# Kernel tuning notes

Measured on AMD Instinct MI355X. Metric: run time of the kernel, lower is better.

## Reference

```python
import jax, jax.numpy as jnp
import numpy as np

SOS = 1

def _gru_cell(x, h, Wih, Whh, bih, bhh):
    # PyTorch GRU cell: gates ordered (r, z, n)
    gi = x @ Wih.T + bih
    gh = h @ Whh.T + bhh
    ir, iz, inn = jnp.split(gi, 3, axis=-1)
    hr, hz, hn = jnp.split(gh, 3, axis=-1)
    r = jax.nn.sigmoid(ir + hr)
    z = jax.nn.sigmoid(iz + hz)
    n = jnp.tanh(inn + r * hn)
    return (1.0 - z) * n + z * h


def setup_inputs() -> dict:
    key = jax.random.key(0)
    ks = jax.random.split(key, 17)
    V, E, H, Lin, Tout, B, Lmax = 50000, 512, 512, 400, 100, 64, 400
    s = 0.05
    f = jax.random.normal
    return {
        "emb":     f(ks[0], (V, E)) * s,
        "enc_Wih": f(ks[1], (3 * H, E)) * s,
        "enc_Whh": f(ks[2], (3 * H, H)) * s,
        "enc_bih": f(ks[3], (3 * H,)) * s,
        "enc_bhh": f(ks[4], (3 * H,)) * s,
        "attn_W":  f(ks[5], (Lmax, 2 * H)) * s,
        "attn_b":  f(ks[6], (Lmax,)) * s,
        "comb_W":  f(ks[7], (H, 2 * H)) * s,
        "comb_b":  f(ks[8], (H,)) * s,
        "dec_Wih": f(ks[9], (3 * H, H)) * s,
        "dec_Whh": f(ks[10], (3 * H, H)) * s,
        "dec_bih": f(ks[11], (3 * H,)) * s,
        "dec_bhh": f(ks[12], (3 * H,)) * s,
        "out_W":   f(ks[13], (V, H)) * s,
        "out_b":   f(ks[14], (V,)) * s,
        "input_tensor":  jax.random.randint(ks[15], (Lin, B), 0, V),
        "target_tensor": jax.random.randint(ks[16], (Tout, B), 0, V),
    }


def reference(emb, enc_Wih, enc_Whh, enc_bih, enc_bhh, attn_W, attn_b,
              comb_W, comb_b, dec_Wih, dec_Whh, dec_bih, dec_bhh,
              out_W, out_b, input_tensor, target_tensor):
    B = input_tensor.shape[1]
    H = enc_Whh.shape[1]

    # ---- encoder: 1-layer GRU over [L, B, E] ----
    enc_x = emb[input_tensor]                      # [L, B, E]
    h0 = jnp.zeros((B, H), enc_x.dtype)
    def enc_step(h, x):
        h2 = _gru_cell(x, h, enc_Wih, enc_Whh, enc_bih, enc_bhh)
        return h2, h2
    h_enc, enc_out = jax.lax.scan(enc_step, h0, enc_x)   # enc_out: [L, B, H]
    enc0 = enc_out[0]                              # [B, H]; source's attn_applied[0] picks timestep 0

    # ---- decoder: teacher-forced, NLLLoss(mean) summed over steps ----
    dec_tokens = jnp.concatenate(
        [jnp.full((1, B), SOS, target_tensor.dtype), target_tensor[:-1]], axis=0)
    dec_x = emb[dec_tokens]                        # [T, B, H] (embed_size == hidden_size)

    def dec_step(h, xt):
        x, tgt = xt                                # x: [B, H], tgt: [B]
        a = jax.nn.softmax(jnp.concatenate([x, h], 1) @ attn_W.T + attn_b, axis=1)  # [B, Lmax]
        # faithful to source: elementwise broadcast picks enc_out[0] scaled by a[:, 0]
        ctx = enc0 * a[:, :1]                      # [B, H]
        c = jax.nn.relu(jnp.concatenate([x, ctx], 1) @ comb_W.T + comb_b)           # [B, H]
        h2 = _gru_cell(c, h, dec_Wih, dec_Whh, dec_bih, dec_bhh)
        logp = jax.nn.log_softmax(h2 @ out_W.T + out_b, axis=1)                     # [B, V]
        loss_t = -jnp.mean(jnp.take_along_axis(logp, tgt[:, None], axis=1))
        return h2, loss_t

    _, losses = jax.lax.scan(dec_step, h_enc, (dec_x, target_tensor))
    return jnp.sum(losses)
```

## Files before the change

### kernel.cpp

```cpp
#include <hip/hip_runtime.h>
#include <math.h>


typedef __attribute__((ext_vector_type(8))) short bh8;
typedef __attribute__((ext_vector_type(4))) float fv4;

__device__ __forceinline__ float b2f(short u) {
    union { unsigned int i; float f; } c;
    c.i = ((unsigned int)(unsigned short)u) << 16;
    return c.f;
}
__device__ __forceinline__ short f2b(float f) {
    union { float f; unsigned int u; } c;
    c.f = f;
    unsigned int r = (c.u + 0x7fffu + ((c.u >> 16) & 1u)) >> 16;
    return (short)r;
}
__device__ __forceinline__ bh8 ld8(const float* __restrict__ p) {
    bh8 r;
    #pragma unroll
    for (int j = 0; j < 8; ++j) r[j] = f2b(p[j]);
    return r;
}
__device__ __forceinline__ float sigmf(float x) { return 1.f / (1.f + expf(-x)); }

__device__ __forceinline__ fv4 mfma16(bh8 a, bh8 b, fv4 c) {
    return __builtin_amdgcn_mfma_f32_16x16x32_bf16(a, b, c, 0, 0, 0);
}

__device__ __forceinline__ void gridbar(unsigned int* bar, unsigned int target) {
    __syncthreads();
    if (threadIdx.x == 0) {
        __hip_atomic_fetch_add(bar, 1u, __ATOMIC_ACQ_REL, __HIP_MEMORY_SCOPE_AGENT);
        while (__hip_atomic_load(bar, __ATOMIC_ACQUIRE, __HIP_MEMORY_SCOPE_AGENT) < target) {
            __builtin_amdgcn_s_sleep(2);
        }
    }
    __syncthreads();
}

__global__ __launch_bounds__(256) void k_cvt(
    const float* __restrict__ s, short* __restrict__ d, int n)
{
    const int i = (blockIdx.x * 256 + threadIdx.x) * 4;
    if (i + 3 < n) {
        fv4 v = *(const fv4*)(s + i);
        short4 o;
        o.x = f2b(v[0]); o.y = f2b(v[1]); o.z = f2b(v[2]); o.w = f2b(v[3]);
        *(short4*)(d + i) = o;
    }
}

__global__ __launch_bounds__(256) void k_enc_persist(
    const float* __restrict__ emb, const int* __restrict__ input_t,
    const short* __restrict__ Wb,
    const float* __restrict__ Wih_f, const float* __restrict__ Whh_f,
    const float* __restrict__ bih, const float* __restrict__ bhh,
    float* __restrict__ h_f32, short* __restrict__ h_bf,
    float* __restrict__ enc0, unsigned int* __restrict__ bar)
{
    const int tid  = threadIdx.x;
    const int lane = tid & 63;
    const int wv   = tid >> 6;
    const int n0   = blockIdx.x * 16;
    const int b0   = wv * 16;
    const int l15  = lane & 15;
    const int ko   = lane >> 4;
    const int koff = ko * 8;
    const int brow = b0 + l15;
    const int n    = n0 + l15;

    for (int i = blockIdx.x * 256 + tid; i < 64 * 512; i += 32 * 256) {
        h_f32[i] = 0.f; h_bf[i] = 0;
    }
    gridbar(bar, 32u);

    const bh8 *Wrb = nullptr, *Wzb = nullptr, *Wnb = nullptr;
    const bh8 *Urb = nullptr, *Uzb = nullptr, *Unb = nullptr;
    const float *Wrf = nullptr, *Wzf = nullptr, *Wnf = nullptr;
    const float *Urf = nullptr, *Uzf = nullptr, *Unf = nullptr;
    if (Wb) {
        Wrb = (const bh8*)(Wb + (long long)(n + 0)    * 512) + ko;
        Wzb = (const bh8*)(Wb + (long long)(n + 512)  * 512) + ko;
        Wnb = (const bh8*)(Wb + (long long)(n + 1024) * 512) + ko;
        Urb = (const bh8*)(Wb + (long long)(n + 1536) * 512) + ko;
        Uzb = (const bh8*)(Wb + (long long)(n + 2048) * 512) + ko;
        Unb = (const bh8*)(Wb + (long long)(n + 2560) * 512) + ko;
    } else {
        Wrf = Wih_f + (long long)(n + 0)    * 512 + koff;
        Wzf = Wih_f + (long long)(n + 512)  * 512 + koff;
        Wnf = Wih_f + (long long)(n + 1024) * 512 + koff;
        Urf = Whh_f + (long long)(n + 0)    * 512 + koff;
        Uzf = Whh_f + (long long)(n + 512)  * 512 + koff;
        Unf = Whh_f + (long long)(n + 1024) * 512 + koff;
    }
    const float bir = bih[n], biz = bih[n + 512], bin = bih[n + 1024];
    const float bhr = bhh[n], bhz = bhh[n + 512], bhn = bhh[n + 1024];

    for (int t = 0; t < 400; ++t) {
        const float* hi  = h_f32 + (t & 1) * 32768;
        const short* hib = h_bf  + (t & 1) * 32768;
        float* ho  = h_f32 + ((t + 1) & 1) * 32768;
        short* hob = h_bf  + ((t + 1) & 1) * 32768;

        const int tok = input_t[t * 64 + brow];
        const float* Ap = emb + (long long)tok * 512 + koff;
        const bh8*  Hp  = (const bh8*)(hib + (long long)brow * 512) + ko;

        fv4 air = {0.f, 0.f, 0.f, 0.f};
        fv4 aiz = air, ain = air, ahr = air, ahz = air, ahn = air;
        if (Wb) {
            #pragma unroll 4
            for (int kk = 0; kk < 16; ++kk) {
                const bh8 a = ld8(Ap + kk * 32);
                const bh8 h = Hp[kk * 4];
                air = mfma16(a, Wrb[kk * 4], air);
                aiz = mfma16(a, Wzb[kk * 4], aiz);
                ain = mfma16(a, Wnb[kk * 4], ain);
                ahr = mfma16(h, Urb[kk * 4], ahr);
                ahz = mfma16(h, Uzb[kk * 4], ahz);
                ahn = mfma16(h, Unb[kk * 4], ahn);
            }
        } else {
            #pragma unroll 4
            for (int kk = 0; kk < 16; ++kk) {
                const bh8 a = ld8(Ap + kk * 32);
                const bh8 h = Hp[kk * 4];
                air = mfma16(a, ld8(Wrf + kk * 32), air);
                aiz = mfma16(a, ld8(Wzf + kk * 32), aiz);
                ain = mfma16(a, ld8(Wnf + kk * 32), ain);
                ahr = mfma16(h, ld8(Urf + kk * 32), ahr);
                ahz = mfma16(h, ld8(Uzf + kk * 32), ahz);
                ahn = mfma16(h, ld8(Unf + kk * 32), ahn);
            }
        }
        #pragma unroll
        for (int r = 0; r < 4; ++r) {
            const int b = b0 + ko * 4 + r;
            const float rr = sigmf(air[r] + bir + ahr[r] + bhr);
            const float zz = sigmf(aiz[r] + biz + ahz[r] + bhz);
            const float nn = tanhf(ain[r] + bin + rr * (ahn[r] + bhn));
            const float hold = hi[b * 512 + n];
            const float hnew = (1.f - zz) * nn + zz * hold;
            ho[b * 512 + n] = hnew;
            hob[b * 512 + n] = f2b(hnew);
            if (t == 0) enc0[b * 512 + n] = hnew;
        }
        gridbar(bar, 32u * (t + 2));
    }
}

__global__ __launch_bounds__(256) void k_gru1(
    const short* __restrict__ c_bf, const short* __restrict__ Wb,
    const float* __restrict__ Wih_f, const float* __restrict__ Whh_f,
    const float* __restrict__ bih, const float* __restrict__ bhh,
    const float* __restrict__ hi, const short* __restrict__ hib,
    float* __restrict__ ho, short* __restrict__ hob)
{
    const int tid  = threadIdx.x;
    const int lane = tid & 63;
    const int w    = blockIdx.x * 4 + (tid >> 6);
    const int b0   = (w & 3) * 16;
    const int n0   = (w >> 2) * 16;
    const int l15  = lane & 15;
    const int ko   = lane >> 4;
    const int koff = ko * 8;
    const int brow = b0 + l15;
    const int n    = n0 + l15;

    const bh8* Ap = (const bh8*)(c_bf + (long long)brow * 512) + ko;
    const bh8* Hp = (const bh8*)(hib + (long long)brow * 512) + ko;

    fv4 air = {0.f, 0.f, 0.f, 0.f};
    fv4 aiz = air, ain = air, ahr = air, ahz = air, ahn = air;
    if (Wb) {
        const bh8* Wr = (const bh8*)(Wb + (long long)(n + 0)    * 512) + ko;
        const bh8* Wz = (const bh8*)(Wb + (long long)(n + 512)  * 512) + ko;
        const bh8* Wn = (const bh8*)(Wb + (long long)(n + 1024) * 512) + ko;
        const bh8* Ur = (const bh8*)(Wb + (long long)(n + 1536) * 512) + ko;
        const bh8* Uz = (const bh8*)(Wb + (long long)(n + 2048) * 512) + ko;
        const bh8* Un = (const bh8*)(Wb + (long long)(n + 2560) * 512) + ko;
        #pragma unroll 4
        for (int kk = 0; kk < 16; ++kk) {
            const bh8 a = Ap[kk * 4];
            const bh8 h = Hp[kk * 4];
            air = mfma16(a, Wr[kk * 4], air);
            aiz = mfma16(a, Wz[kk * 4], aiz);
            ain = mfma16(a, Wn[kk * 4], ain);
            ahr = mfma16(h, Ur[kk * 4], ahr);
            ahz = mfma16(h, Uz[kk * 4], ahz);
            ahn = mfma16(h, Un[kk * 4], ahn);
        }
    } else {
        const float* Wr = Wih_f + (long long)(n + 0)    * 512 + koff;
        const float* Wz = Wih_f + (long long)(n + 512)  * 512 + koff;
        const float* Wn = Wih_f + (long long)(n + 1024) * 512 + koff;
        const float* Ur = Whh_f + (long long)(n + 0)    * 512 + koff;
        const float* Uz = Whh_f + (long long)(n + 512)  * 512 + koff;
        const float* Un = Whh_f + (long long)(n + 1024) * 512 + koff;
        #pragma unroll 4
        for (int kk = 0; kk < 16; ++kk) {
            const bh8 a = Ap[kk * 4];
            const bh8 h = Hp[kk * 4];
            air = mfma16(a, ld8(Wr + kk * 32), air);
            aiz = mfma16(a, ld8(Wz + kk * 32), aiz);
            ain = mfma16(a, ld8(Wn + kk * 32), ain);
            ahr = mfma16(h, ld8(Ur + kk * 32), ahr);
            ahz = mfma16(h, ld8(Uz + kk * 32), ahz);
            ahn = mfma16(h, ld8(Un + kk * 32), ahn);
        }
    }
    const float bir = bih[n], biz = bih[n + 512], bin = bih[n + 1024];
    const float bhr = bhh[n], bhz = bhh[n + 512], bhn = bhh[n + 1024];
    #pragma unroll
    for (int r = 0; r < 4; ++r) {
        const int b = b0 + ko * 4 + r;
        const float rr = sigmf(air[r] + bir + ahr[r] + bhr);
        const float zz = sigmf(aiz[r] + biz + ahz[r] + bhz);
        const float nn = tanhf(ain[r] + bin + rr * (ahn[r] + bhn));
        const float hold = hi[b * 512 + n];
        const float hnew = (1.f - zz) * nn + zz * hold;
        ho[b * 512 + n] = hnew;
        hob[b * 512 + n] = f2b(hnew);
    }
}

__global__ __launch_bounds__(256) void k_attncomb(
    const float* __restrict__ emb, const float* __restrict__ h_f32,
    const float* __restrict__ enc0,
    const float* __restrict__ attn_W, const float* __restrict__ attn_b,
    const float* __restrict__ comb_W, const float* __restrict__ comb_b,
    const int* __restrict__ target, int td, short* __restrict__ c_bf)
{
    __shared__ float sx[1024];
    __shared__ float sc[400];
    __shared__ float red[256];
    __shared__ float a0s;
    const int b = blockIdx.x;
    const int tid = threadIdx.x;
    const int tok = (td == 0) ? 1 : target[(td - 1) * 64 + b];
    for (int k = tid; k < 512; k += 256) {
        sx[k] = emb[(long long)tok * 512 + k];
        sx[512 + k] = h_f32[b * 512 + k];
    }
    __syncthreads();
    for (int nn = tid; nn < 400; nn += 256) {
        const fv4* wrow = (const fv4*)(attn_W + (long long)nn * 1024);
        float acc = 0.f;
        for (int kc = 0; kc < 256; ++kc) {
            fv4 v = wrow[kc];
            acc += v[0] * sx[kc * 4 + 0] + v[1] * sx[kc * 4 + 1]
                 + v[2] * sx[kc * 4 + 2] + v[3] * sx[kc * 4 + 3];
        }
        sc[nn] = acc + attn_b[nn];
    }
    __syncthreads();
    float m = -1e30f;
    for (int nn = tid; nn < 400; nn += 256) m = fmaxf(m, sc[nn]);
    red[tid] = m;
    __syncthreads();
    for (int s = 128; s > 0; s >>= 1) {
        if (tid < s) red[tid] = fmaxf(red[tid], red[tid + s]);
        __syncthreads();
    }
    m = red[0];
    __syncthreads();
    float ss = 0.f;
    for (int nn = tid; nn < 400; nn += 256) ss += expf(sc[nn] - m);
    red[tid] = ss;
    __syncthreads();
    for (int s = 128; s > 0; s >>= 1) {
        if (tid < s) red[tid] += red[tid + s];
        __syncthreads();
    }
    if (tid == 0) a0s = expf(sc[0] - m) / red[0];
    __syncthreads();
    const float a0b = a0s;
    for (int k = tid; k < 512; k += 256) sx[512 + k] = enc0[b * 512 + k] * a0b;
    __syncthreads();
    for (int j = tid; j < 512; j += 256) {
        const fv4* wrow = (const fv4*)(comb_W + (long long)j * 1024);
        float acc = 0.f;
        for (int kc = 0; kc < 256; ++kc) {
            fv4 v = wrow[kc];
            acc += v[0] * sx[kc * 4 + 0] + v[1] * sx[kc * 4 + 1]
                 + v[2] * sx[kc * 4 + 2] + v[3] * sx[kc * 4 + 3];
        }
        acc += comb_b[j];
        c_bf[b * 512 + j] = f2b(fmaxf(acc, 0.f));
    }
}

__global__ __launch_bounds__(256) void k_outloss(
    const short* __restrict__ h2bf,
    const short* __restrict__ outWb, const float* __restrict__ outW,
    const float* __restrict__ outb, const int* __restrict__ target,
    float* __restrict__ pm, float* __restrict__ ps, float* __restrict__ tlogit)
{
    __shared__ float sl[64][65];
    const int tid  = threadIdx.x;
    const int lane = tid & 63;
    const int wl   = tid >> 6;
    const int base = blockIdx.x * 64;
    const int n0   = base + wl * 16;
    const int l15  = lane & 15;
    const int ko   = lane >> 4;

    const int v    = n0 + l15;
    const int vcl  = (v < 50000) ? v : 49999;
    const bh8* A0 = (const bh8*)(h2bf + (long long)(0  + l15) * 512) + ko;
    const bh8* A1 = (const bh8*)(h2bf + (long long)(16 + l15) * 512) + ko;
    const bh8* A2 = (const bh8*)(h2bf + (long long)(32 + l15) * 512) + ko;
    const bh8* A3 = (const bh8*)(h2bf + (long long)(48 + l15) * 512) + ko;
    fv4 c0 = {0.f, 0.f, 0.f, 0.f};
    fv4 c1 = c0, c2 = c0, c3 = c0;
    if (outWb) {
        const bh8* Bp = (const bh8*)(outWb + (long long)vcl * 512) + ko;
        #pragma unroll 4
        for (int kk = 0; kk < 16; ++kk) {
            const bh8 bb = Bp[kk * 4];
            c0 = mfma16(A0[kk * 4], bb, c0);
            c1 = mfma16(A1[kk * 4], bb, c1);
            c2 = mfma16(A2[kk * 4], bb, c2);
            c3 = mfma16(A3[kk * 4], bb, c3);
        }
    } else {
        const float* Bp = outW + (long long)vcl * 512 + ko * 8;
        #pragma unroll 4
        for (int kk = 0; kk < 16; ++kk) {
            const bh8 bb = ld8(Bp + kk * 32);
            c0 = mfma16(A0[kk * 4], bb, c0);
            c1 = mfma16(A1[kk * 4], bb, c1);
            c2 = mfma16(A2[kk * 4], bb, c2);
            c3 = mfma16(A3[kk * 4], bb, c3);
        }
    }
    const float bv = outb[vcl];
    const int cc = wl * 16 + l15;
    const bool ok = (v < 50000);
    #pragma unroll
    for (int r = 0; r < 4; ++r) {
        const int row = ko * 4 + r;
        sl[0  + row][cc] = ok ? (c0[r] + bv) : -1e30f;
        sl[16 + row][cc] = ok ? (c1[r] + bv) : -1e30f;
        sl[32 + row][cc] = ok ? (c2[r] + bv) : -1e30f;
        sl[48 + row][cc] = ok ? (c3[r] + bv) : -1e30f;
    }
    __syncthreads();
    if (tid < 64) {
        const int b = tid;
        float m = -1e30f, s = 0.f;
        for (int c = 0; c < 64; ++c) {
            const float x = sl[b][c];
            if (x > m) { s = s * expf(m - x) + 1.f; m = x; }
            else       { s += expf(x - m); }
        }
        pm[blockIdx.x * 64 + b] = m;
        ps[blockIdx.x * 64 + b] = s;
        const int tg = target[b];
        const int rel = tg - base;
        if (rel >= 0 && rel < 64) tlogit[b] = sl[b][rel];
    }
}

__global__ __launch_bounds__(256) void k_lossred(
    const float* __restrict__ pm, const float* __restrict__ ps,
    const float* __restrict__ tlogit, float* __restrict__ loss_acc)
{
    __shared__ float rm[256], rs[256];
    const int b = blockIdx.x;
    const int tid = threadIdx.x;
    float m = -1e30f, s = 0.f;
    for (int i = tid; i < 782; i += 256) {
        const float m2 = pm[i * 64 + b];
        const float s2 = ps[i * 64 + b];
        if (m2 > m) { s = s * expf(m - m2) + s2; m = m2; }
        else        { s += s2 * expf(m2 - m); }
    }
    rm[tid] = m; rs[tid] = s;
    __syncthreads();
    for (int st = 128; st > 0; st >>= 1) {
        if (tid < st) {
            const float m2 = rm[tid + st], s2 = rs[tid + st];
            const float M = fmaxf(rm[tid], m2);
            rs[tid] = rs[tid] * expf(rm[tid] - M) + s2 * expf(m2 - M);
            rm[tid] = M;
        }
        __syncthreads();
    }
    if (tid == 0) {
        const float logp = tlogit[b] - (rm[0] + logf(rs[0]));
        atomicAdd(loss_acc, -logp * (1.f / 64.f));
    }
}

__global__ void k_init(float* h_f32_0, short* h_bf_0, float* loss_acc,
                       unsigned int* bar)
{
    const int i = blockIdx.x * 256 + threadIdx.x;
    if (i < 64 * 512) { h_f32_0[i] = 0.f; h_bf_0[i] = 0; }
    if (i == 0) { *loss_acc = 0.f; *bar = 0u; }
}

__global__ void k_final(const float* loss_acc, float* out)
{
    out[0] = *loss_acc;
}

extern "C" void kernel_launch(void* const* d_in, const int* in_sizes, int n_in,
                              void* d_out, int out_size, void* d_ws, size_t ws_size,
                              hipStream_t stream)
{
    const float* emb     = (const float*)d_in[0];
    const float* enc_Wih = (const float*)d_in[1];
    const float* enc_Whh = (const float*)d_in[2];
    const float* enc_bih = (const float*)d_in[3];
    const float* enc_bhh = (const float*)d_in[4];
    const float* attn_W  = (const float*)d_in[5];
    const float* attn_b  = (const float*)d_in[6];
    const float* comb_W  = (const float*)d_in[7];
    const float* comb_b  = (const float*)d_in[8];
    const float* dec_Wih = (const float*)d_in[9];
    const float* dec_Whh = (const float*)d_in[10];
    const float* dec_bih = (const float*)d_in[11];
    const float* dec_bhh = (const float*)d_in[12];
    const float* out_W   = (const float*)d_in[13];
    const float* out_b   = (const float*)d_in[14];
    const int*   input_t = (const int*)d_in[15];
    const int*   target_t= (const int*)d_in[16];

    char* ws = (char*)d_ws;
    float* h_f32  = (float*)(ws + 0);
    float* enc0   = (float*)(ws + 262144);
    short* h_bf   = (short*)(ws + 393216);
    short* c_bf   = (short*)(ws + 524288);
    float* lacc   = (float*)(ws + 589824);
    unsigned int* bar = (unsigned int*)(ws + 590080);
    float* pm     = (float*)(ws + 590336);
    float* ps     = (float*)(ws + 790528);
    float* tlog   = (float*)(ws + 990720);
    short* encWb  = (short*)(ws + 990976);
    short* decWb  = (short*)(ws + 4136704);
    short* outWb  = (short*)(ws + 7282432);

    const bool tier1 = ws_size >= 7282432;
    const bool tier2 = ws_size >= 58482432;

    k_init<<<128, 256, 0, stream>>>(h_f32, h_bf, lacc, bar);

    if (tier1) {
        k_cvt<<<768, 256, 0, stream>>>(enc_Wih, encWb, 786432);
        k_cvt<<<768, 256, 0, stream>>>(enc_Whh, encWb + 786432, 786432);
        k_cvt<<<768, 256, 0, stream>>>(dec_Wih, decWb, 786432);
        k_cvt<<<768, 256, 0, stream>>>(dec_Whh, decWb + 786432, 786432);
    }
    if (tier2) {
        k_cvt<<<25000, 256, 0, stream>>>(out_W, outWb, 25600000);
    }

    k_enc_persist<<<32, 256, 0, stream>>>(
        emb, input_t, tier1 ? encWb : nullptr, enc_Wih, enc_Whh,
        enc_bih, enc_bhh, h_f32, h_bf, enc0, bar);

    for (int td = 0; td < 100; ++td) {
        const float* hi  = h_f32 + (td & 1) * 32768;
        const short* hib = h_bf  + (td & 1) * 32768;
        float* ho  = h_f32 + ((td + 1) & 1) * 32768;
        short* hob = h_bf  + ((td + 1) & 1) * 32768;
        k_attncomb<<<64, 256, 0, stream>>>(emb, hi, enc0, attn_W, attn_b,
                                           comb_W, comb_b, target_t, td, c_bf);
        k_gru1<<<32, 256, 0, stream>>>(c_bf, tier1 ? decWb : nullptr,
                                       dec_Wih, dec_Whh, dec_bih, dec_bhh,
                                       hi, hib, ho, hob);
        k_outloss<<<782, 256, 0, stream>>>(hob, tier2 ? outWb : nullptr, out_W,
                                           out_b, target_t + td * 64,
                                           pm, ps, tlog);
        k_lossred<<<64, 256, 0, stream>>>(pm, ps, tlog, lacc);
    }

    k_final<<<1, 1, 0, stream>>>(lacc, (float*)d_out);
}
```

Baseline: 28.86 ms.

## Fuse decoder steps into a single persistent kernel with grid barriers

Replaces the per-step launches of the attention/combine, GRU, output-projection and loss-reduction kernels with one persistent 256-block kernel that loops over all 100 decoder steps, separating phases with grid-wide barriers. The loss reduction of step t is folded into the start of step t+1, and attention scores are staged in reused workspace. This removes hundreds of kernel launches and their gaps, at the cost of fewer blocks per phase and a dependence on all blocks being co-resident for the barriers.

```diff
diff --git a/kernel.cpp b/kernel.cpp
--- a/kernel.cpp
+++ b/kernel.cpp
@@ -148,6 +148,272 @@
         }
         gridbar(bar, 32u * (t + 2));
     }
+}
+
+struct SmAB { float sx[1024]; float red[256]; float red2[256]; };
+struct SmD  { float sl[64][65]; };
+union SMem { SmAB ab; SmD d; };
+
+__device__ __forceinline__ void dec_lossred(
+    const float* __restrict__ pm, const float* __restrict__ ps,
+    const float* __restrict__ tlog, float* __restrict__ lacc,
+    float* red, float* red2, int r, int tid)
+{
+    float m = -1e30f, s = 0.f;
+    for (int i = tid; i < 782; i += 256) {
+        const float m2 = pm[i * 64 + r];
+        const float s2 = ps[i * 64 + r];
+        if (m2 > m) { s = s * expf(m - m2) + s2; m = m2; }
+        else        { s += s2 * expf(m2 - m); }
+    }
+    red[tid] = m; red2[tid] = s;
+    __syncthreads();
+    for (int st = 128; st > 0; st >>= 1) {
+        if (tid < st) {
+            const float m2 = red[tid + st], s2 = red2[tid + st];
+            const float M = fmaxf(red[tid], m2);
+            red2[tid] = red2[tid] * expf(red[tid] - M) + s2 * expf(m2 - M);
+            red[tid] = M;
+        }
+        __syncthreads();
+    }
+    if (tid == 0) {
+        const float logp = tlog[r] - (red[0] + logf(red2[0]));
+        atomicAdd(lacc, -logp * (1.f / 64.f));
+    }
+    __syncthreads();
+}
+
+__global__ __launch_bounds__(256) void k_dec_persist(
+    const float* __restrict__ emb, const float* __restrict__ enc0,
+    const float* __restrict__ attn_W, const float* __restrict__ attn_b,
+    const float* __restrict__ comb_W, const float* __restrict__ comb_b,
+    const short* __restrict__ decWb,
+    const float* __restrict__ dec_Wih, const float* __restrict__ dec_Whh,
+    const float* __restrict__ dec_bih, const float* __restrict__ dec_bhh,
+    const short* __restrict__ outWb, const float* __restrict__ outW,
+    const float* __restrict__ outb, const int* __restrict__ target,
+    float* __restrict__ h_f32, short* __restrict__ h_bf,
+    short* __restrict__ c_bf, float* __restrict__ scores,
+    float* __restrict__ pm, float* __restrict__ ps,
+    float* __restrict__ tlog, float* __restrict__ lacc,
+    unsigned int* __restrict__ bar2)
+{
+    __shared__ SMem sm;
+    const int tid = threadIdx.x;
+    const int bid = blockIdx.x;
+    const int r   = bid >> 2;
+    const int q   = bid & 3;
+    unsigned int tgt = 0u;
+
+    for (int t = 0; t < 100; ++t) {
+        const float* hi  = h_f32 + (t & 1) * 32768;
+        const short* hib = h_bf  + (t & 1) * 32768;
+        float* ho  = h_f32 + ((t + 1) & 1) * 32768;
+        short* hob = h_bf  + ((t + 1) & 1) * 32768;
+
+        const int tok = (t == 0) ? 1 : target[(t - 1) * 64 + r];
+        for (int k = tid; k < 512; k += 256) {
+            sm.ab.sx[k]       = emb[(long long)tok * 512 + k];
+            sm.ab.sx[512 + k] = hi[r * 512 + k];
+        }
+        if (q == 0 && t > 0)
+            dec_lossred(pm, ps, tlog, lacc, sm.ab.red, sm.ab.red2, r, tid);
+        __syncthreads();
+        if (tid < 100) {
+            const int nn = q * 100 + tid;
+            const fv4* wrow = (const fv4*)(attn_W + (long long)nn * 1024);
+            float s0 = 0.f, s1 = 0.f, s2 = 0.f, s3 = 0.f;
+            for (int kc = 0; kc < 256; ++kc) {
+                fv4 v = wrow[kc];
+                s0 += v[0] * sm.ab.sx[kc * 4 + 0];
+                s1 += v[1] * sm.ab.sx[kc * 4 + 1];
+                s2 += v[2] * sm.ab.sx[kc * 4 + 2];
+                s3 += v[3] * sm.ab.sx[kc * 4 + 3];
+            }
+            scores[r * 400 + nn] = (s0 + s1) + (s2 + s3) + attn_b[nn];
+        }
+        tgt += 256u; gridbar(bar2, tgt);
+
+        {
+            float m = -1e30f;
+            for (int i = tid; i < 400; i += 256) m = fmaxf(m, scores[r * 400 + i]);
+            sm.ab.red[tid] = m;
+            __syncthreads();
+            for (int st = 128; st > 0; st >>= 1) {
+                if (tid < st) sm.ab.red[tid] = fmaxf(sm.ab.red[tid], sm.ab.red[tid + st]);
+                __syncthreads();
+            }
+            m = sm.ab.red[0];
+            __syncthreads();
+            float ssum = 0.f;
+            for (int i = tid; i < 400; i += 256) ssum += expf(scores[r * 400 + i] - m);
+            sm.ab.red2[tid] = ssum;
+            __syncthreads();
+            for (int st = 128; st > 0; st >>= 1) {
+                if (tid < st) sm.ab.red2[tid] += sm.ab.red2[tid + st];
+                __syncthreads();
+            }
+            const float a0 = expf(scores[r * 400 + 0] - m) / sm.ab.red2[0];
+            __syncthreads();
+            for (int k = tid; k < 512; k += 256)
+                sm.ab.sx[512 + k] = enc0[r * 512 + k] * a0;
+            __syncthreads();
+        }
+        if (tid < 128) {
+            const int j = q * 128 + tid;
+            const fv4* wrow = (const fv4*)(comb_W + (long long)j * 1024);
+            float s0 = 0.f, s1 = 0.f, s2 = 0.f, s3 = 0.f;
+            for (int kc = 0; kc < 256; ++kc) {
+                fv4 v = wrow[kc];
+                s0 += v[0] * sm.ab.sx[kc * 4 + 0];
+                s1 += v[1] * sm.ab.sx[kc * 4 + 1];
+                s2 += v[2] * sm.ab.sx[kc * 4 + 2];
+                s3 += v[3] * sm.ab.sx[kc * 4 + 3];
+            }
+            const float acc = (s0 + s1) + (s2 + s3) + comb_b[j];
+            c_bf[r * 512 + j] = f2b(fmaxf(acc, 0.f));
+        }
+        tgt += 256u; gridbar(bar2, tgt);
+
+        if (bid < 32) {
+            const int lane = tid & 63;
+            const int w    = bid * 4 + (tid >> 6);
+            const int b0g  = (w & 3) * 16;
+            const int n0g  = (w >> 2) * 16;
+            const int l15  = lane & 15;
+            const int ko   = lane >> 4;
+            const int koff = ko * 8;
+            const int brow = b0g + l15;
+            const int n    = n0g + l15;
+
+            const bh8* Ap = (const bh8*)(c_bf + (long long)brow * 512) + ko;
+            const bh8* Hp = (const bh8*)(hib + (long long)brow * 512) + ko;
+
+            fv4 air = {0.f, 0.f, 0.f, 0.f};
+            fv4 aiz = air, ain = air, ahr = air, ahz = air, ahn = air;
+            if (decWb) {
+                const bh8* Wr = (const bh8*)(decWb + (long long)(n + 0)    * 512) + ko;
+                const bh8* Wz = (const bh8*)(decWb + (long long)(n + 512)  * 512) + ko;
+                const bh8* Wn = (const bh8*)(decWb + (long long)(n + 1024) * 512) + ko;
+                const bh8* Ur = (const bh8*)(decWb + (long long)(n + 1536) * 512) + ko;
+                const bh8* Uz = (const bh8*)(decWb + (long long)(n + 2048) * 512) + ko;
+                const bh8* Un = (const bh8*)(decWb + (long long)(n + 2560) * 512) + ko;
+                #pragma unroll 4
+                for (int kk = 0; kk < 16; ++kk) {
+                    const bh8 a = Ap[kk * 4];
+                    const bh8 h = Hp[kk * 4];
+                    air = mfma16(a, Wr[kk * 4], air);
+                    aiz = mfma16(a, Wz[kk * 4], aiz);
+                    ain = mfma16(a, Wn[kk * 4], ain);
+                    ahr = mfma16(h, Ur[kk * 4], ahr);
+                    ahz = mfma16(h, Uz[kk * 4], ahz);
+                    ahn = mfma16(h, Un[kk * 4], ahn);
+                }
+            } else {
+                const float* Wr = dec_Wih + (long long)(n + 0)    * 512 + koff;
+                const float* Wz = dec_Wih + (long long)(n + 512)  * 512 + koff;
+                const float* Wn = dec_Wih + (long long)(n + 1024) * 512 + koff;
+                const float* Ur = dec_Whh + (long long)(n + 0)    * 512 + koff;
+                const float* Uz = dec_Whh + (long long)(n + 512)  * 512 + koff;
+                const float* Un = dec_Whh + (long long)(n + 1024) * 512 + koff;
+                #pragma unroll 4
+                for (int kk = 0; kk < 16; ++kk) {
+                    const bh8 a = Ap[kk * 4];
+                    const bh8 h = Hp[kk * 4];
+                    air = mfma16(a, ld8(Wr + kk * 32), air);
+                    aiz = mfma16(a, ld8(Wz + kk * 32), aiz);
+                    ain = mfma16(a, ld8(Wn + kk * 32), ain);
+                    ahr = mfma16(h, ld8(Ur + kk * 32), ahr);
+                    ahz = mfma16(h, ld8(Uz + kk * 32), ahz);
+                    ahn = mfma16(h, ld8(Un + kk * 32), ahn);
+                }
+            }
+            const float bir = dec_bih[n], biz = dec_bih[n + 512], bin = dec_bih[n + 1024];
+            const float bhr = dec_bhh[n], bhz = dec_bhh[n + 512], bhn = dec_bhh[n + 1024];
+            #pragma unroll
+            for (int rr = 0; rr < 4; ++rr) {
+                const int b = b0g + ko * 4 + rr;
+                const float rg = sigmf(air[rr] + bir + ahr[rr] + bhr);
+                const float zg = sigmf(aiz[rr] + biz + ahz[rr] + bhz);
+                const float ng = tanhf(ain[rr] + bin + rg * (ahn[rr] + bhn));
+                const float hold = hi[b * 512 + n];
+                const float hnew = (1.f - zg) * ng + zg * hold;
+                ho[b * 512 + n] = hnew;
+                hob[b * 512 + n] = f2b(hnew);
+            }
+        }
+        tgt += 256u; gridbar(bar2, tgt);
+
+        for (int ch = bid; ch < 782; ch += 256) {
+            const int lane = tid & 63;
+            const int wl   = tid >> 6;
+            const int base = ch * 64;
+            const int n0c  = base + wl * 16;
+            const int l15  = lane & 15;
+            const int ko   = lane >> 4;
+            const int v    = n0c + l15;
+            const int vcl  = (v < 50000) ? v : 49999;
+            const bh8* A0 = (const bh8*)(hob + (long long)(0  + l15) * 512) + ko;
+            const bh8* A1 = (const bh8*)(hob + (long long)(16 + l15) * 512) + ko;
+            const bh8* A2 = (const bh8*)(hob + (long long)(32 + l15) * 512) + ko;
+            const bh8* A3 = (const bh8*)(hob + (long long)(48 + l15) * 512) + ko;
+            fv4 c0 = {0.f, 0.f, 0.f, 0.f};
+            fv4 c1 = c0, c2 = c0, c3 = c0;
+            if (outWb) {
+                const bh8* Bp = (const bh8*)(outWb + (long long)vcl * 512) + ko;
+                #pragma unroll 4
+                for (int kk = 0; kk < 16; ++kk) {
+                    const bh8 bb = Bp[kk * 4];
+                    c0 = mfma16(A0[kk * 4], bb, c0);
+                    c1 = mfma16(A1[kk * 4], bb, c1);
+                    c2 = mfma16(A2[kk * 4], bb, c2);
+                    c3 = mfma16(A3[kk * 4], bb, c3);
+                }
+            } else {
+                const float* Bp = outW + (long long)vcl * 512 + ko * 8;
+                #pragma unroll 4
+                for (int kk = 0; kk < 16; ++kk) {
+                    const bh8 bb = ld8(Bp + kk * 32);
+                    c0 = mfma16(A0[kk * 4], bb, c0);
+                    c1 = mfma16(A1[kk * 4], bb, c1);
+                    c2 = mfma16(A2[kk * 4], bb, c2);
+                    c3 = mfma16(A3[kk * 4], bb, c3);
+                }
+            }
+            const float bv = outb[vcl];
+            const int cc = wl * 16 + l15;
+            const bool ok = (v < 50000);
+            #pragma unroll
+            for (int rr = 0; rr < 4; ++rr) {
+                const int row = ko * 4 + rr;
+                sm.d.sl[0  + row][cc] = ok ? (c0[rr] + bv) : -1e30f;
+                sm.d.sl[16 + row][cc] = ok ? (c1[rr] + bv) : -1e30f;
+                sm.d.sl[32 + row][cc] = ok ? (c2[rr] + bv) : -1e30f;
+                sm.d.sl[48 + row][cc] = ok ? (c3[rr] + bv) : -1e30f;
+            }
+            __syncthreads();
+            if (tid < 64) {
+                const int b = tid;
+                float m = -1e30f, s = 0.f;
+                for (int cj = 0; cj < 64; ++cj) {
+                    const float x = sm.d.sl[b][cj];
+                    if (x > m) { s = s * expf(m - x) + 1.f; m = x; }
+                    else       { s += expf(x - m); }
+                }
+                pm[ch * 64 + b] = m;
+                ps[ch * 64 + b] = s;
+                const int tg = target[t * 64 + b];
+                const int rel = tg - base;
+                if (rel >= 0 && rel < 64) tlog[b] = sm.d.sl[b][rel];
+            }
+            __syncthreads();
+        }
+        tgt += 256u; gridbar(bar2, tgt);
+    }
+
+    if (q == 0)
+        dec_lossred(pm, ps, tlog, lacc, sm.ab.red, sm.ab.red2, r, tid);
 }
 
 __global__ __launch_bounds__(256) void k_gru1(
@@ -395,11 +661,11 @@
 }
 
 __global__ void k_init(float* h_f32_0, short* h_bf_0, float* loss_acc,
-                       unsigned int* bar)
+                       unsigned int* bar, unsigned int* bar2)
 {
     const int i = blockIdx.x * 256 + threadIdx.x;
     if (i < 64 * 512) { h_f32_0[i] = 0.f; h_bf_0[i] = 0; }
-    if (i == 0) { *loss_acc = 0.f; *bar = 0u; }
+    if (i == 0) { *loss_acc = 0.f; *bar = 0u; *bar2 = 0u; }
 }
 
 __global__ void k_final(const float* loss_acc, float* out)
@@ -435,18 +701,21 @@
     short* h_bf   = (short*)(ws + 393216);
     short* c_bf   = (short*)(ws + 524288);
     float* lacc   = (float*)(ws + 589824);
-    unsigned int* bar = (unsigned int*)(ws + 590080);
+    unsigned int* bar  = (unsigned int*)(ws + 590080);
+    unsigned int* bar2 = (unsigned int*)(ws + 590208);
     float* pm     = (float*)(ws + 590336);
     float* ps     = (float*)(ws + 790528);
     float* tlog   = (float*)(ws + 990720);
     short* encWb  = (short*)(ws + 990976);
+    float* scores = (float*)(ws + 990976);
     short* decWb  = (short*)(ws + 4136704);
     short* outWb  = (short*)(ws + 7282432);
 
     const bool tier1 = ws_size >= 7282432;
     const bool tier2 = ws_size >= 58482432;
-
-    k_init<<<128, 256, 0, stream>>>(h_f32, h_bf, lacc, bar);
+    const bool fuse  = ws_size >= 1093376;
+
+    k_init<<<128, 256, 0, stream>>>(h_f32, h_bf, lacc, bar, bar2);
 
     if (tier1) {
         k_cvt<<<768, 256, 0, stream>>>(enc_Wih, encWb, 786432);
@@ -462,20 +731,28 @@
         emb, input_t, tier1 ? encWb : nullptr, enc_Wih, enc_Whh,
         enc_bih, enc_bhh, h_f32, h_bf, enc0, bar);
 
-    for (int td = 0; td < 100; ++td) {
-        const float* hi  = h_f32 + (td & 1) * 32768;
-        const short* hib = h_bf  + (td & 1) * 32768;
-        float* ho  = h_f32 + ((td + 1) & 1) * 32768;
-        short* hob = h_bf  + ((td + 1) & 1) * 32768;
-        k_attncomb<<<64, 256, 0, stream>>>(emb, hi, enc0, attn_W, attn_b,
-                                           comb_W, comb_b, target_t, td, c_bf);
-        k_gru1<<<32, 256, 0, stream>>>(c_bf, tier1 ? decWb : nullptr,
-                                       dec_Wih, dec_Whh, dec_bih, dec_bhh,
-                                       hi, hib, ho, hob);
-        k_outloss<<<782, 256, 0, stream>>>(hob, tier2 ? outWb : nullptr, out_W,
-                                           out_b, target_t + td * 64,
-                                           pm, ps, tlog);
-        k_lossred<<<64, 256, 0, stream>>>(pm, ps, tlog, lacc);
+    if (fuse) {
+        k_dec_persist<<<256, 256, 0, stream>>>(
+            emb, enc0, attn_W, attn_b, comb_W, comb_b,
+            tier1 ? decWb : nullptr, dec_Wih, dec_Whh, dec_bih, dec_bhh,
+            tier2 ? outWb : nullptr, out_W, out_b, target_t,
+            h_f32, h_bf, c_bf, scores, pm, ps, tlog, lacc, bar2);
+    } else {
+        for (int td = 0; td < 100; ++td) {
+            const float* hi  = h_f32 + (td & 1) * 32768;
+            const short* hib = h_bf  + (td & 1) * 32768;
+            float* ho  = h_f32 + ((td + 1) & 1) * 32768;
+            short* hob = h_bf  + ((td + 1) & 1) * 32768;
+            k_attncomb<<<64, 256, 0, stream>>>(emb, hi, enc0, attn_W, attn_b,
+                                               comb_W, comb_b, target_t, td, c_bf);
+            k_gru1<<<32, 256, 0, stream>>>(c_bf, tier1 ? decWb : nullptr,
+                                           dec_Wih, dec_Whh, dec_bih, dec_bhh,
+                                           hi, hib, ho, hob);
+            k_outloss<<<782, 256, 0, stream>>>(hob, tier2 ? outWb : nullptr, out_W,
+                                               out_b, target_t + td * 64,
+                                               pm, ps, tlog);
+            k_lossred<<<64, 256, 0, stream>>>(pm, ps, tlog, lacc);
+        }
     }
 
     k_final<<<1, 1, 0, stream>>>(lacc, (float*)d_out);
```

After: 32.56 ms. +12.8%, slower.
